# Kernel optimization log

Hardware: AMD Instinct MI355X
Metric: run time of the kernel (lower is better)

Reference implementation:

```python
import jax, jax.numpy as jnp
import numpy as np

N_NODES = 50000
N_EDGES = 800000
HDIM = 256
NUMRELS = 16


def setup_inputs() -> dict:
    key = jax.random.key(0)
    ks = jax.random.split(key, 9)
    h = jax.random.normal(ks[0], (N_NODES, HDIM), dtype=jnp.float32)
    relvectors = jax.random.normal(ks[1], (NUMRELS, HDIM), dtype=jnp.float32)
    # GRUCell params (torch layout: [3*hdim, hdim] rows = [r, z, n])
    s = 1.0 / np.sqrt(HDIM)
    w_ih = jax.random.uniform(ks[2], (3 * HDIM, HDIM), minval=-s, maxval=s, dtype=jnp.float32)
    w_hh = jax.random.uniform(ks[3], (3 * HDIM, HDIM), minval=-s, maxval=s, dtype=jnp.float32)
    b_ih = jax.random.uniform(ks[4], (3 * HDIM,), minval=-s, maxval=s, dtype=jnp.float32)
    b_hh = jax.random.uniform(ks[5], (3 * HDIM,), minval=-s, maxval=s, dtype=jnp.float32)
    edge_src = jax.random.randint(ks[6], (N_EDGES,), 0, N_NODES, dtype=jnp.int32)
    edge_dst = jax.random.randint(ks[7], (N_EDGES,), 0, N_NODES, dtype=jnp.int32)
    edge_rel = jax.random.randint(ks[8], (N_EDGES,), 0, NUMRELS, dtype=jnp.int32)
    return {"h": h, "relvectors": relvectors, "w_ih": w_ih, "w_hh": w_hh,
            "b_ih": b_ih, "b_hh": b_hh, "edge_src": edge_src,
            "edge_dst": edge_dst, "edge_rel": edge_rel}


def _gru_cell(x, h, w_ih, w_hh, b_ih, b_hh):
    # torch.nn.GRUCell semantics
    gi = x @ w_ih.T + b_ih  # [N, 3H]
    gh = h @ w_hh.T + b_hh  # [N, 3H]
    i_r, i_z, i_n = jnp.split(gi, 3, axis=-1)
    h_r, h_z, h_n = jnp.split(gh, 3, axis=-1)
    r = jax.nn.sigmoid(i_r + h_r)
    z = jax.nn.sigmoid(i_z + h_z)
    n = jnp.tanh(i_n + r * h_n)
    return (1.0 - z) * n + z * h


def reference(h, relvectors, w_ih, w_hh, b_ih, b_hh, edge_src, edge_dst, edge_rel):
    # message: per-edge gather of source node state + relation vector by edge id
    msg = h[edge_src] + relvectors[edge_rel]          # [E, H]
    # reduce: segment-sum over destination nodes (mailbox sum)
    red = jax.ops.segment_sum(msg, edge_dst, num_segments=h.shape[0])  # [N, H]
    # apply: GRUCell node update (input=red, hidden=h)
    return _gru_cell(red, h, w_ih, w_hh, b_ih, b_hh)
```

## Files before the change

kernel.cpp:

```cpp
#include <hip/hip_runtime.h>

#define H 256

typedef __attribute__((ext_vector_type(8))) short short8;
typedef __attribute__((ext_vector_type(8))) unsigned short ushort8v;
typedef __attribute__((ext_vector_type(16))) float f32x16;

__device__ __forceinline__ ushort f2bf(float f) {
  unsigned u = __float_as_uint(f);
  unsigned r = (u + 0x7fffu + ((u >> 16) & 1u)) >> 16;
  return (ushort)r;
}
__device__ __forceinline__ float bf2f(ushort s) {
  return __uint_as_float(((unsigned)s) << 16);
}
__device__ __forceinline__ void gld_lds16(const void* g, void* lds) {
  __builtin_amdgcn_global_load_lds(
      (const __attribute__((address_space(1))) unsigned int*)g,
      (__attribute__((address_space(3))) unsigned int*)lds, 16, 0, 0);
}

__global__ void k_cvt(const float* __restrict__ src, ushort* __restrict__ dst, int n4) {
  int i = blockIdx.x * blockDim.x + threadIdx.x;
  if (i < n4) {
    float4 f = *(const float4*)&src[(size_t)i * 4];
    ushort4 o;
    o.x = f2bf(f.x); o.y = f2bf(f.y); o.z = f2bf(f.z); o.w = f2bf(f.w);
    *(ushort4*)&dst[(size_t)i * 4] = o;
  }
}

__global__ void k_zero(int* cnt, int n) {
  int i = blockIdx.x * blockDim.x + threadIdx.x;
  if (i < n) cnt[i] = 0;
}

__global__ void k_hist(const int* __restrict__ dst, int* __restrict__ cnt, int ne) {
  int e = blockIdx.x * blockDim.x + threadIdx.x;
  if (e < ne) atomicAdd(&cnt[dst[e]], 1);
}

__global__ __launch_bounds__(256) void k_scan1(const int* __restrict__ cnt,
                                               int* __restrict__ bsum, int n) {
  __shared__ int s[256];
  int t = threadIdx.x, i = blockIdx.x * 256 + t;
  int v = (i < n) ? cnt[i] : 0;
  s[t] = v;
  __syncthreads();
  for (int o = 128; o > 0; o >>= 1) {
    if (t < o) s[t] += s[t + o];
    __syncthreads();
  }
  if (t == 0) bsum[blockIdx.x] = s[0];
}

__global__ __launch_bounds__(256) void k_scan2(const int* __restrict__ bsum,
                                               int* __restrict__ bpre, int nb,
                                               int* __restrict__ offs, int n) {
  __shared__ int s[256];
  int t = threadIdx.x;
  int v = (t < nb) ? bsum[t] : 0;
  s[t] = v;
  __syncthreads();
  for (int o = 1; o < 256; o <<= 1) {
    int x = (t >= o) ? s[t - o] : 0;
    __syncthreads();
    s[t] += x;
    __syncthreads();
  }
  if (t < nb) bpre[t] = s[t] - v;
  if (t == 255) offs[n] = s[255];
}

__global__ __launch_bounds__(256) void k_scan3(const int* __restrict__ cnt,
                                               const int* __restrict__ bpre,
                                               int* __restrict__ offs,
                                               int* __restrict__ cursor, int n) {
  __shared__ int s[256];
  int t = threadIdx.x, i = blockIdx.x * 256 + t;
  int v = (i < n) ? cnt[i] : 0;
  s[t] = v;
  __syncthreads();
  for (int o = 1; o < 256; o <<= 1) {
    int x = (t >= o) ? s[t - o] : 0;
    __syncthreads();
    s[t] += x;
    __syncthreads();
  }
  if (i < n) {
    int e = bpre[blockIdx.x] + s[t] - v;
    offs[i] = e;
    cursor[i] = e;
  }
}

__global__ void k_fill(const int* __restrict__ src, const int* __restrict__ dst,
                       const int* __restrict__ rel, int* __restrict__ cursor,
                       int* __restrict__ bucket, int ne) {
  int e = blockIdx.x * blockDim.x + threadIdx.x;
  if (e < ne) {
    int p = atomicAdd(&cursor[dst[e]], 1);
    bucket[p] = src[e] | (rel[e] << 16);
  }
}

__global__ __launch_bounds__(256) void k_gather(const ushort* __restrict__ h16,
                                                const float* __restrict__ relv,
                                                const int* __restrict__ offs,
                                                const int* __restrict__ bucket,
                                                ushort* __restrict__ red16, int nn) {
  const int hw = threadIdx.x >> 5;
  const int l = threadIdx.x & 31;
  const int node = blockIdx.x * 8 + hw;
  if (node >= nn) return;
  const int beg = offs[node], end = offs[node + 1];
  float acc[8] = {0.f, 0.f, 0.f, 0.f, 0.f, 0.f, 0.f, 0.f};
  int i = beg;
  for (; i + 2 <= end; i += 2) {
    const int p0 = bucket[i], p1 = bucket[i + 1];
    const ushort8v a0 = *(const ushort8v*)&h16[(size_t)(p0 & 0xFFFF) * H + l * 8];
    const ushort8v a1 = *(const ushort8v*)&h16[(size_t)(p1 & 0xFFFF) * H + l * 8];
    const float4 r0a = *(const float4*)&relv[(p0 >> 16) * H + l * 8];
    const float4 r0b = *(const float4*)&relv[(p0 >> 16) * H + l * 8 + 4];
    const float4 r1a = *(const float4*)&relv[(p1 >> 16) * H + l * 8];
    const float4 r1b = *(const float4*)&relv[(p1 >> 16) * H + l * 8 + 4];
    acc[0] += bf2f(a0[0]) + r0a.x + bf2f(a1[0]) + r1a.x;
    acc[1] += bf2f(a0[1]) + r0a.y + bf2f(a1[1]) + r1a.y;
    acc[2] += bf2f(a0[2]) + r0a.z + bf2f(a1[2]) + r1a.z;
    acc[3] += bf2f(a0[3]) + r0a.w + bf2f(a1[3]) + r1a.w;
    acc[4] += bf2f(a0[4]) + r0b.x + bf2f(a1[4]) + r1b.x;
    acc[5] += bf2f(a0[5]) + r0b.y + bf2f(a1[5]) + r1b.y;
    acc[6] += bf2f(a0[6]) + r0b.z + bf2f(a1[6]) + r1b.z;
    acc[7] += bf2f(a0[7]) + r0b.w + bf2f(a1[7]) + r1b.w;
  }
  if (i < end) {
    const int p0 = bucket[i];
    const ushort8v a0 = *(const ushort8v*)&h16[(size_t)(p0 & 0xFFFF) * H + l * 8];
    const float4 r0a = *(const float4*)&relv[(p0 >> 16) * H + l * 8];
    const float4 r0b = *(const float4*)&relv[(p0 >> 16) * H + l * 8 + 4];
    acc[0] += bf2f(a0[0]) + r0a.x;
    acc[1] += bf2f(a0[1]) + r0a.y;
    acc[2] += bf2f(a0[2]) + r0a.z;
    acc[3] += bf2f(a0[3]) + r0a.w;
    acc[4] += bf2f(a0[4]) + r0b.x;
    acc[5] += bf2f(a0[5]) + r0b.y;
    acc[6] += bf2f(a0[6]) + r0b.z;
    acc[7] += bf2f(a0[7]) + r0b.w;
  }
  ushort8v o;
#pragma unroll
  for (int e = 0; e < 8; ++e) o[e] = f2bf(acc[e]);
  *(ushort8v*)&red16[(size_t)node * H + l * 8] = o;
}

__global__ __launch_bounds__(512, 2) void k_gru_mfma(
    const ushort* __restrict__ red16, const ushort* __restrict__ h16,
    const float* __restrict__ hmat,
    const ushort* __restrict__ wih16, const ushort* __restrict__ whh16,
    const float* __restrict__ b_ih, const float* __restrict__ b_hh,
    float* __restrict__ out, int nn) {
  __shared__ unsigned char smem[81920];
  const int tid = threadIdx.x;
  const int wid = tid >> 6;
  const int lane = tid & 63;
  const int l31 = lane & 31;
  const int lhi = lane >> 5;
  const int row0 = blockIdx.x * 128;
  const int hcol0 = blockIdx.y * 64;

  const int fA = wid * 64 + lane;
  const int A_kg2hi = fA >> 7;
  const int A_row = fA & 127;
  int A_grow = row0 + A_row;
  if (A_grow >= nn) A_grow = nn - 1;
  const size_t A_srcoff = (size_t)A_grow * H + (A_kg2hi >> 1) * 16 + (A_kg2hi & 1) * 8;
  const ushort* W_mat[3];
  size_t W_srcoff[3];
  for (int jj = 0; jj < 3; ++jj) {
    const int f = (wid * 3 + jj) * 64 + lane;
    const int kg2hi = f / 384;
    const int gcol = f % 384;
    const int sg = gcol >> 6, cis = gcol & 63;
    W_mat[jj] = (sg < 3) ? wih16 : whh16;
    const int gate = (sg < 3) ? sg : sg - 3;
    W_srcoff[jj] = (size_t)(gate * 256 + hcol0 + cis) * H + (kg2hi >> 1) * 16 + (kg2hi & 1) * 8;
  }

#define STAGE(bufo, kb) do { \
    const int kboff = (kb) * 32; \
    gld_lds16(red16 + A_srcoff + kboff, &smem[(bufo) + wid * 1024]); \
    gld_lds16(h16 + A_srcoff + kboff, &smem[(bufo) + 8192 + wid * 1024]); \
    gld_lds16(W_mat[0] + W_srcoff[0] + kboff, &smem[(bufo) + 16384 + (wid * 3 + 0) * 1024]); \
    gld_lds16(W_mat[1] + W_srcoff[1] + kboff, &smem[(bufo) + 16384 + (wid * 3 + 1) * 1024]); \
    gld_lds16(W_mat[2] + W_srcoff[2] + kboff, &smem[(bufo) + 16384 + (wid * 3 + 2) * 1024]); \
  } while (0)

  f32x16 acc[2][3] = {};
  const int mato = (wid >= 4) ? 8192 : 0;
  const int sgb = (wid >= 4) ? 3 : 0;
  const int R0 = ((wid >> 1) & 1) * 64;
  const int C = (wid & 1) * 32;

  STAGE(0, 0);
  __syncthreads();
  for (int kb = 0; kb < 8; ++kb) {
    const int bo = (kb & 1) * 40960;
    if (kb < 7) STAGE(40960 - bo, kb + 1);
#pragma unroll
    for (int kg = 0; kg < 2; ++kg) {
      const int ko = kg * 2 + lhi;
      const short8 a0 = *(const short8*)&smem[bo + mato + ko * 2048 + (R0 + l31) * 16];
      const short8 a1 = *(const short8*)&smem[bo + mato + ko * 2048 + (R0 + 32 + l31) * 16];
      const short8 b0 = *(const short8*)&smem[bo + 16384 + ko * 6144 + ((sgb + 0) * 64 + C + l31) * 16];
      const short8 b1 = *(const short8*)&smem[bo + 16384 + ko * 6144 + ((sgb + 1) * 64 + C + l31) * 16];
      const short8 b2 = *(const short8*)&smem[bo + 16384 + ko * 6144 + ((sgb + 2) * 64 + C + l31) * 16];
      acc[0][0] = __builtin_amdgcn_mfma_f32_32x32x16_bf16(a0, b0, acc[0][0], 0, 0, 0);
      acc[0][1] = __builtin_amdgcn_mfma_f32_32x32x16_bf16(a0, b1, acc[0][1], 0, 0, 0);
      acc[0][2] = __builtin_amdgcn_mfma_f32_32x32x16_bf16(a0, b2, acc[0][2], 0, 0, 0);
      acc[1][0] = __builtin_amdgcn_mfma_f32_32x32x16_bf16(a1, b0, acc[1][0], 0, 0, 0);
      acc[1][1] = __builtin_amdgcn_mfma_f32_32x32x16_bf16(a1, b1, acc[1][1], 0, 0, 0);
      acc[1][2] = __builtin_amdgcn_mfma_f32_32x32x16_bf16(a1, b2, acc[1][2], 0, 0, 0);
    }
    __syncthreads();
  }
#undef STAGE

  if (wid >= 4) {
    const int ww = wid - 4;
#pragma unroll
    for (int rt = 0; rt < 2; ++rt)
#pragma unroll
      for (int s = 0; s < 3; ++s) {
        ushort tmp[16];
#pragma unroll
        for (int r = 0; r < 16; ++r) tmp[r] = f2bf(acc[rt][s][r]);
        const int so = ww * 12288 + (rt * 3 + s) * 2048 + lane * 32;
        *(ushort8v*)&smem[so] = *(const ushort8v*)&tmp[0];
        *(ushort8v*)&smem[so + 16] = *(const ushort8v*)&tmp[8];
      }
  }
  __syncthreads();

  if (wid < 4) {
    const int hcol = hcol0 + C + l31;
    const float bir = b_ih[hcol], biz = b_ih[256 + hcol], bin = b_ih[512 + hcol];
    const float bhr = b_hh[hcol], bhz = b_hh[256 + hcol], bhn = b_hh[512 + hcol];
#pragma unroll
    for (int rt = 0; rt < 2; ++rt) {
      ushort hr_[16], hz_[16], hn_[16];
      const int so = wid * 12288 + rt * 3 * 2048 + lane * 32;
      *(ushort8v*)&hr_[0] = *(const ushort8v*)&smem[so];
      *(ushort8v*)&hr_[8] = *(const ushort8v*)&smem[so + 16];
      *(ushort8v*)&hz_[0] = *(const ushort8v*)&smem[so + 2048];
      *(ushort8v*)&hz_[8] = *(const ushort8v*)&smem[so + 2048 + 16];
      *(ushort8v*)&hn_[0] = *(const ushort8v*)&smem[so + 4096];
      *(ushort8v*)&hn_[8] = *(const ushort8v*)&smem[so + 4096 + 16];
#pragma unroll
      for (int r = 0; r < 16; ++r) {
        const int rowc = (r & 3) + 8 * (r >> 2) + 4 * lhi;
        const int grow = row0 + R0 + rt * 32 + rowc;
        if (grow < nn) {
          const float ir_ = acc[rt][0][r] + bir;
          const float iz_ = acc[rt][1][r] + biz;
          const float in_ = acc[rt][2][r] + bin;
          const float hr = bf2f(hr_[r]) + bhr;
          const float hz = bf2f(hz_[r]) + bhz;
          const float hn = bf2f(hn_[r]) + bhn;
          const float rg = 1.f / (1.f + __expf(-(ir_ + hr)));
          const float zg = 1.f / (1.f + __expf(-(iz_ + hz)));
          const float ng = tanhf(in_ + rg * hn);
          const float hv = hmat[(size_t)grow * H + hcol];
          out[(size_t)grow * H + hcol] = (1.f - zg) * ng + zg * hv;
        }
      }
    }
  }
}

extern "C" void kernel_launch(void* const* d_in, const int* in_sizes, int n_in,
                              void* d_out, int out_size, void* d_ws, size_t ws_size,
                              hipStream_t stream) {
  const float* h    = (const float*)d_in[0];
  const float* relv = (const float*)d_in[1];
  const float* w_ih = (const float*)d_in[2];
  const float* w_hh = (const float*)d_in[3];
  const float* b_ih = (const float*)d_in[4];
  const float* b_hh = (const float*)d_in[5];
  const int* esrc   = (const int*)d_in[6];
  const int* edst   = (const int*)d_in[7];
  const int* erel   = (const int*)d_in[8];
  float* out = (float*)d_out;
  const int nn = in_sizes[0] / H;
  const int ne = in_sizes[6];
  const int nw = in_sizes[2];
  const int nb = (nn + 255) / 256;

  char* w = (char*)d_ws;
  ushort* red16 = (ushort*)w;  w += (size_t)nn * H * 2;
  ushort* h16   = (ushort*)w;  w += (size_t)nn * H * 2;
  ushort* wih16 = (ushort*)w;  w += (size_t)nw * 2;
  ushort* whh16 = (ushort*)w;  w += (size_t)nw * 2;
  int* cnt    = (int*)w;       w += (size_t)nn * 4;
  int* offs   = (int*)w;       w += (size_t)(nn + 4) * 4;
  int* cursor = (int*)w;       w += (size_t)nn * 4;
  int* bsum   = (int*)w;       w += 256 * 4;
  int* bpre   = (int*)w;       w += 256 * 4;
  int* bucket = (int*)w;

  k_cvt<<<(nn * H / 4 + 255) / 256, 256, 0, stream>>>(h, h16, nn * H / 4);
  k_cvt<<<(nw / 4 + 255) / 256, 256, 0, stream>>>(w_ih, wih16, nw / 4);
  k_cvt<<<(nw / 4 + 255) / 256, 256, 0, stream>>>(w_hh, whh16, nw / 4);

  k_zero<<<(nn + 255) / 256, 256, 0, stream>>>(cnt, nn);
  k_hist<<<(ne + 255) / 256, 256, 0, stream>>>(edst, cnt, ne);
  k_scan1<<<nb, 256, 0, stream>>>(cnt, bsum, nn);
  k_scan2<<<1, 256, 0, stream>>>(bsum, bpre, nb, offs, nn);
  k_scan3<<<nb, 256, 0, stream>>>(cnt, bpre, offs, cursor, nn);
  k_fill<<<(ne + 255) / 256, 256, 0, stream>>>(esrc, edst, erel, cursor, bucket, ne);

  k_gather<<<(nn + 7) / 8, 256, 0, stream>>>(h16, relv, offs, bucket, red16, nn);

  dim3 grid((nn + 127) / 128, 4);
  k_gru_mfma<<<grid, 512, 0, stream>>>(red16, h16, h, wih16, whh16, b_ih, b_hh, out, nn);
}
```

Before: 443.3 us.

## Pre-tile activations and weights into fragment-major layout, load MFMA operands directly

The conversion kernels and the gather now write bf16 activations and weights in a panel/fragment-major layout that matches the MFMA operand pattern. The GRU GEMM kernel then drops its LDS double-buffered staging and barriers and loads operands straight from global memory. LDS use shrinks, leaving only the epilogue exchange. The cost is an extra row-major copy of h and reliance on L2/L1 hits for operand reuse across waves, since each wave now fetches its fragments independently.

```diff
diff --git a/kernel.cpp b/kernel.cpp
--- a/kernel.cpp
+++ b/kernel.cpp
@@ -14,20 +14,33 @@
 __device__ __forceinline__ float bf2f(ushort s) {
   return __uint_as_float(((unsigned)s) << 16);
 }
-__device__ __forceinline__ void gld_lds16(const void* g, void* lds) {
-  __builtin_amdgcn_global_load_lds(
-      (const __attribute__((address_space(1))) unsigned int*)g,
-      (__attribute__((address_space(3))) unsigned int*)lds, 16, 0, 0);
-}
-
-__global__ void k_cvt(const float* __restrict__ src, ushort* __restrict__ dst, int n4) {
-  int i = blockIdx.x * blockDim.x + threadIdx.x;
-  if (i < n4) {
-    float4 f = *(const float4*)&src[(size_t)i * 4];
-    ushort4 o;
-    o.x = f2bf(f.x); o.y = f2bf(f.y); o.z = f2bf(f.z); o.w = f2bf(f.w);
-    *(ushort4*)&dst[(size_t)i * 4] = o;
-  }
+
+
+__global__ void k_cvt_h(const float* __restrict__ src, ushort* __restrict__ h16row,
+                        ushort* __restrict__ hfm, int nrows) {
+  int t = blockIdx.x * blockDim.x + threadIdx.x;
+  if (t >= nrows * 32) return;
+  const int row = t >> 5, l = t & 31;
+  const float4 fa = *(const float4*)&src[(size_t)row * H + l * 8];
+  const float4 fb = *(const float4*)&src[(size_t)row * H + l * 8 + 4];
+  ushort8v o;
+  o[0] = f2bf(fa.x); o[1] = f2bf(fa.y); o[2] = f2bf(fa.z); o[3] = f2bf(fa.w);
+  o[4] = f2bf(fb.x); o[5] = f2bf(fb.y); o[6] = f2bf(fb.z); o[7] = f2bf(fb.w);
+  *(ushort8v*)&h16row[(size_t)row * H + l * 8] = o;
+  const int p = row >> 7, r = row & 127;
+  *(ushort8v*)((char*)hfm + (size_t)p * 65536 + (size_t)l * 2048 + r * 16) = o;
+}
+
+__global__ void k_cvt_w(const float* __restrict__ w, ushort* __restrict__ wfm, int gbase) {
+  int t = blockIdx.x * blockDim.x + threadIdx.x;
+  if (t >= 768 * 32) return;
+  const int j = t >> 5, l = t & 31;
+  const float4 fa = *(const float4*)&w[(size_t)j * H + l * 8];
+  const float4 fb = *(const float4*)&w[(size_t)j * H + l * 8 + 4];
+  ushort8v o;
+  o[0] = f2bf(fa.x); o[1] = f2bf(fa.y); o[2] = f2bf(fa.z); o[3] = f2bf(fa.w);
+  o[4] = f2bf(fb.x); o[5] = f2bf(fb.y); o[6] = f2bf(fb.z); o[7] = f2bf(fb.w);
+  *(ushort8v*)((char*)wfm + ((size_t)l * 1536 + gbase + j) * 16) = o;
 }
 
 __global__ void k_zero(int* cnt, int n) {
@@ -108,7 +121,7 @@
                                                 const float* __restrict__ relv,
                                                 const int* __restrict__ offs,
                                                 const int* __restrict__ bucket,
-                                                ushort* __restrict__ red16, int nn) {
+                                                ushort* __restrict__ redfm, int nn) {
   const int hw = threadIdx.x >> 5;
   const int l = threadIdx.x & 31;
   const int node = blockIdx.x * 8 + hw;
@@ -150,16 +163,16 @@
   ushort8v o;
 #pragma unroll
   for (int e = 0; e < 8; ++e) o[e] = f2bf(acc[e]);
-  *(ushort8v*)&red16[(size_t)node * H + l * 8] = o;
+  const int p = node >> 7, r = node & 127;
+  *(ushort8v*)((char*)redfm + (size_t)p * 65536 + (size_t)l * 2048 + r * 16) = o;
 }
 
 __global__ __launch_bounds__(512, 2) void k_gru_mfma(
-    const ushort* __restrict__ red16, const ushort* __restrict__ h16,
-    const float* __restrict__ hmat,
-    const ushort* __restrict__ wih16, const ushort* __restrict__ whh16,
+    const ushort* __restrict__ redfm, const ushort* __restrict__ hfm,
+    const float* __restrict__ hmat, const ushort* __restrict__ wfm,
     const float* __restrict__ b_ih, const float* __restrict__ b_hh,
     float* __restrict__ out, int nn) {
-  __shared__ unsigned char smem[81920];
+  __shared__ unsigned char smem[49152];
   const int tid = threadIdx.x;
   const int wid = tid >> 6;
   const int lane = tid & 63;
@@ -167,53 +180,27 @@
   const int lhi = lane >> 5;
   const int row0 = blockIdx.x * 128;
   const int hcol0 = blockIdx.y * 64;
-
-  const int fA = wid * 64 + lane;
-  const int A_kg2hi = fA >> 7;
-  const int A_row = fA & 127;
-  int A_grow = row0 + A_row;
-  if (A_grow >= nn) A_grow = nn - 1;
-  const size_t A_srcoff = (size_t)A_grow * H + (A_kg2hi >> 1) * 16 + (A_kg2hi & 1) * 8;
-  const ushort* W_mat[3];
-  size_t W_srcoff[3];
-  for (int jj = 0; jj < 3; ++jj) {
-    const int f = (wid * 3 + jj) * 64 + lane;
-    const int kg2hi = f / 384;
-    const int gcol = f % 384;
-    const int sg = gcol >> 6, cis = gcol & 63;
-    W_mat[jj] = (sg < 3) ? wih16 : whh16;
-    const int gate = (sg < 3) ? sg : sg - 3;
-    W_srcoff[jj] = (size_t)(gate * 256 + hcol0 + cis) * H + (kg2hi >> 1) * 16 + (kg2hi & 1) * 8;
-  }
-
-#define STAGE(bufo, kb) do { \
-    const int kboff = (kb) * 32; \
-    gld_lds16(red16 + A_srcoff + kboff, &smem[(bufo) + wid * 1024]); \
-    gld_lds16(h16 + A_srcoff + kboff, &smem[(bufo) + 8192 + wid * 1024]); \
-    gld_lds16(W_mat[0] + W_srcoff[0] + kboff, &smem[(bufo) + 16384 + (wid * 3 + 0) * 1024]); \
-    gld_lds16(W_mat[1] + W_srcoff[1] + kboff, &smem[(bufo) + 16384 + (wid * 3 + 1) * 1024]); \
-    gld_lds16(W_mat[2] + W_srcoff[2] + kboff, &smem[(bufo) + 16384 + (wid * 3 + 2) * 1024]); \
-  } while (0)
-
-  f32x16 acc[2][3] = {};
-  const int mato = (wid >= 4) ? 8192 : 0;
-  const int sgb = (wid >= 4) ? 3 : 0;
+  const bool is_hh = (wid >= 4);
   const int R0 = ((wid >> 1) & 1) * 64;
   const int C = (wid & 1) * 32;
 
-  STAGE(0, 0);
-  __syncthreads();
+  const char* amat = (const char*)(is_hh ? hfm : redfm);
+  const char* wbase = (const char*)wfm;
+  const size_t a_base = (size_t)blockIdx.x * 65536 + (size_t)lhi * 2048 + (size_t)(R0 + l31) * 16;
+  const size_t b_base = (size_t)lhi * 24576 + (size_t)((is_hh ? 768 : 0) + hcol0 + C + l31) * 16;
+
+  f32x16 acc[2][3] = {};
+#pragma unroll 2
   for (int kb = 0; kb < 8; ++kb) {
-    const int bo = (kb & 1) * 40960;
-    if (kb < 7) STAGE(40960 - bo, kb + 1);
 #pragma unroll
     for (int kg = 0; kg < 2; ++kg) {
-      const int ko = kg * 2 + lhi;
-      const short8 a0 = *(const short8*)&smem[bo + mato + ko * 2048 + (R0 + l31) * 16];
-      const short8 a1 = *(const short8*)&smem[bo + mato + ko * 2048 + (R0 + 32 + l31) * 16];
-      const short8 b0 = *(const short8*)&smem[bo + 16384 + ko * 6144 + ((sgb + 0) * 64 + C + l31) * 16];
-      const short8 b1 = *(const short8*)&smem[bo + 16384 + ko * 6144 + ((sgb + 1) * 64 + C + l31) * 16];
-      const short8 b2 = *(const short8*)&smem[bo + 16384 + ko * 6144 + ((sgb + 2) * 64 + C + l31) * 16];
+      const size_t ao = a_base + (size_t)(kb * 8192 + kg * 4096);
+      const size_t bo = b_base + (size_t)(kb * 4 + kg * 2) * 24576;
+      const short8 a0 = *(const short8*)(amat + ao);
+      const short8 a1 = *(const short8*)(amat + ao + 512);
+      const short8 b0 = *(const short8*)(wbase + bo);
+      const short8 b1 = *(const short8*)(wbase + bo + 4096);
+      const short8 b2 = *(const short8*)(wbase + bo + 8192);
       acc[0][0] = __builtin_amdgcn_mfma_f32_32x32x16_bf16(a0, b0, acc[0][0], 0, 0, 0);
       acc[0][1] = __builtin_amdgcn_mfma_f32_32x32x16_bf16(a0, b1, acc[0][1], 0, 0, 0);
       acc[0][2] = __builtin_amdgcn_mfma_f32_32x32x16_bf16(a0, b2, acc[0][2], 0, 0, 0);
@@ -221,11 +208,9 @@
       acc[1][1] = __builtin_amdgcn_mfma_f32_32x32x16_bf16(a1, b1, acc[1][1], 0, 0, 0);
       acc[1][2] = __builtin_amdgcn_mfma_f32_32x32x16_bf16(a1, b2, acc[1][2], 0, 0, 0);
     }
-    __syncthreads();
-  }
-#undef STAGE
-
-  if (wid >= 4) {
+  }
+
+  if (is_hh) {
     const int ww = wid - 4;
 #pragma unroll
     for (int rt = 0; rt < 2; ++rt)
@@ -241,7 +226,7 @@
   }
   __syncthreads();
 
-  if (wid < 4) {
+  if (!is_hh) {
     const int hcol = hcol0 + C + l31;
     const float bir = b_ih[hcol], biz = b_ih[256 + hcol], bin = b_ih[512 + hcol];
     const float bhr = b_hh[hcol], bhz = b_hh[256 + hcol], bhn = b_hh[512 + hcol];
@@ -292,24 +277,24 @@
   float* out = (float*)d_out;
   const int nn = in_sizes[0] / H;
   const int ne = in_sizes[6];
-  const int nw = in_sizes[2];
+  const int npan = (nn + 127) / 128;
   const int nb = (nn + 255) / 256;
 
   char* w = (char*)d_ws;
-  ushort* red16 = (ushort*)w;  w += (size_t)nn * H * 2;
-  ushort* h16   = (ushort*)w;  w += (size_t)nn * H * 2;
-  ushort* wih16 = (ushort*)w;  w += (size_t)nw * 2;
-  ushort* whh16 = (ushort*)w;  w += (size_t)nw * 2;
-  int* cnt    = (int*)w;       w += (size_t)nn * 4;
-  int* offs   = (int*)w;       w += (size_t)(nn + 4) * 4;
-  int* cursor = (int*)w;       w += (size_t)nn * 4;
-  int* bsum   = (int*)w;       w += 256 * 4;
-  int* bpre   = (int*)w;       w += 256 * 4;
+  ushort* redfm  = (ushort*)w;  w += (size_t)npan * 65536;
+  ushort* hfm    = (ushort*)w;  w += (size_t)npan * 65536;
+  ushort* h16row = (ushort*)w;  w += (size_t)nn * H * 2;
+  ushort* wfm    = (ushort*)w;  w += (size_t)32 * 1536 * 16;
+  int* cnt    = (int*)w;        w += (size_t)nn * 4;
+  int* offs   = (int*)w;        w += (size_t)(nn + 4) * 4;
+  int* cursor = (int*)w;        w += (size_t)nn * 4;
+  int* bsum   = (int*)w;        w += 256 * 4;
+  int* bpre   = (int*)w;        w += 256 * 4;
   int* bucket = (int*)w;
 
-  k_cvt<<<(nn * H / 4 + 255) / 256, 256, 0, stream>>>(h, h16, nn * H / 4);
-  k_cvt<<<(nw / 4 + 255) / 256, 256, 0, stream>>>(w_ih, wih16, nw / 4);
-  k_cvt<<<(nw / 4 + 255) / 256, 256, 0, stream>>>(w_hh, whh16, nw / 4);
+  k_cvt_h<<<(nn * 32 + 255) / 256, 256, 0, stream>>>(h, h16row, hfm, nn);
+  k_cvt_w<<<96, 256, 0, stream>>>(w_ih, wfm, 0);
+  k_cvt_w<<<96, 256, 0, stream>>>(w_hh, wfm, 768);
 
   k_zero<<<(nn + 255) / 256, 256, 0, stream>>>(cnt, nn);
   k_hist<<<(ne + 255) / 256, 256, 0, stream>>>(edst, cnt, ne);
@@ -318,8 +303,8 @@
   k_scan3<<<nb, 256, 0, stream>>>(cnt, bpre, offs, cursor, nn);
   k_fill<<<(ne + 255) / 256, 256, 0, stream>>>(esrc, edst, erel, cursor, bucket, ne);
 
-  k_gather<<<(nn + 7) / 8, 256, 0, stream>>>(h16, relv, offs, bucket, red16, nn);
-
-  dim3 grid((nn + 127) / 128, 4);
-  k_gru_mfma<<<grid, 512, 0, stream>>>(red16, h16, h, wih16, whh16, b_ih, b_hh, out, nn);
-}
+  k_gather<<<(nn + 7) / 8, 256, 0, stream>>>(h16row, relv, offs, bucket, redfm, nn);
+
+  dim3 grid(npan, 4);
+  k_gru_mfma<<<grid, 512, 0, stream>>>(redfm, hfm, h, wfm, b_ih, b_hh, out, nn);
+}
```

Measured after the change: 407.4 us. -8.1%, faster.
